# Kernel optimization log

Hardware: AMD Instinct MI355X
Metric: run time of the kernel (lower is better)

The kernel has to match this reference:

```python
import jax, jax.numpy as jnp
import numpy as np

N_HEAD = 12
LN_EPS = 1e-5


def _layernorm(x, g, b):
    m = jnp.mean(x, axis=-1, keepdims=True)
    v = jnp.mean(jnp.square(x - m), axis=-1, keepdims=True)
    return (x - m) * jax.lax.rsqrt(v + LN_EPS) * g + b


def _block(x, p):
    # p holds single-layer params. x: [B, S, D]
    B, S, D = x.shape
    Dh = D // N_HEAD
    h = _layernorm(x, p['ln1_g'], p['ln1_b'])
    q = (h @ p['wq'] + p['bq']).reshape(B, S, N_HEAD, Dh)
    k = (h @ p['wk'] + p['bk']).reshape(B, S, N_HEAD, Dh)
    v = (h @ p['wv'] + p['bv']).reshape(B, S, N_HEAD, Dh)
    scores = jnp.einsum('bqhd,bkhd->bhqk', q, k) / np.sqrt(Dh).astype(x.dtype)
    causal = jnp.tril(jnp.ones((S, S), dtype=bool))  # valid_nums = arange(1..S)
    scores = jnp.where(causal, scores, -jnp.inf)
    attn = jax.nn.softmax(scores, axis=-1)  # dropout is identity in eval
    o = jnp.einsum('bhqk,bkhd->bqhd', attn, v).reshape(B, S, D)
    x = x + o @ p['wo'] + p['bo']
    h2 = _layernorm(x, p['ln2_g'], p['ln2_b'])
    ff = jax.nn.gelu(h2 @ p['w1'] + p['b1'], approximate=False) @ p['w2'] + p['b2']
    return x + ff


def _gpt_forward(idx, wte, wpe, layer_params, lnf_g, lnf_b, lm_w):
    S = idx.shape[1]
    x = wte[idx] + wpe[None, :S, :]  # embd dropout is identity in eval
    x = jax.lax.scan(lambda c, p: (_block(c, p), None), x, layer_params)[0]
    x = _layernorm(x, lnf_g, lnf_b)
    return x @ lm_w  # logits [B, S, V]


def setup_inputs() -> dict:
    B, S, D, V, L, F = 4, 1024, 768, 50257, 12, 3072
    key = jax.random.key(0)
    ks = iter(jax.random.split(key, 24))
    std = 0.02
    std_proj = 0.02 / np.sqrt(2 * L)  # special init for w_o / FFN.linear2

    def w(shape, s=std):
        return jax.random.normal(next(ks), shape, jnp.float32) * s

    return dict(
        idx=jax.random.randint(next(ks), (B, S), 0, V),
        wte=w((V, D)), wpe=w((S, D)),
        ln1_g=jnp.ones((L, D)), ln1_b=jnp.zeros((L, D)),
        wq=w((L, D, D)), bq=jnp.zeros((L, D)),
        wk=w((L, D, D)), bk=jnp.zeros((L, D)),
        wv=w((L, D, D)), bv=jnp.zeros((L, D)),
        wo=w((L, D, D), std_proj), bo=jnp.zeros((L, D)),
        ln2_g=jnp.ones((L, D)), ln2_b=jnp.zeros((L, D)),
        w1=w((L, D, F)), b1=jnp.zeros((L, F)),
        w2=w((L, F, D), std_proj), b2=jnp.zeros((L, D)),
        lnf_g=jnp.ones((D,)), lnf_b=jnp.zeros((D,)),
        lm_w=w((D, V)),
    )


def reference(idx, wte, wpe, ln1_g, ln1_b, wq, bq, wk, bk, wv, bv, wo, bo,
              ln2_g, ln2_b, w1, b1, w2, b2, lnf_g, lnf_b, lm_w):
    layer_params = dict(ln1_g=ln1_g, ln1_b=ln1_b, wq=wq, bq=bq, wk=wk, bk=bk,
                        wv=wv, bv=bv, wo=wo, bo=bo, ln2_g=ln2_g, ln2_b=ln2_b,
                        w1=w1, b1=b1, w2=w2, b2=b2)
    return _gpt_forward(idx, wte, wpe, layer_params, lnf_g, lnf_b, lm_w)
```

## Files before the change

kernel.cpp:

```cpp
#include <hip/hip_runtime.h>
#include <hip/hip_bf16.h>

typedef __attribute__((ext_vector_type(8))) short short8;
typedef __attribute__((ext_vector_type(4))) float floatx4;

#define GLD16(g, l) __builtin_amdgcn_global_load_lds( \
    (__attribute__((address_space(1))) void*)(g),      \
    (__attribute__((address_space(3))) void*)(l), 16, 0, 0)

#define MFMA_BF16(a, b, c) __builtin_amdgcn_mfma_f32_16x16x32_bf16((a), (b), (c), 0, 0, 0)

__device__ __forceinline__ short f2bf(float f) {
  union { __hip_bfloat16 h; short s; } u;
  u.h = __float2bfloat16(f);
  return u.s;
}

__global__ __launch_bounds__(256)
void transpose_convert(const float* __restrict__ in, short* __restrict__ out,
                       const int K, const int N, const size_t inStride,
                       const size_t outStride) {
  in += blockIdx.z * inStride;
  out += blockIdx.z * outStride;
  __shared__ float tile[32][33];
  const int n0 = blockIdx.x * 32;
  const int k0 = blockIdx.y * 32;
  const int tx = threadIdx.x;
  const int ty = threadIdx.y;
#pragma unroll
  for (int i = 0; i < 4; ++i) {
    const int kk = ty + i * 8;
    const int nn = n0 + tx;
    tile[kk][tx] = (nn < N) ? in[(size_t)(k0 + kk) * N + nn] : 0.f;
  }
  __syncthreads();
#pragma unroll
  for (int i = 0; i < 4; ++i) {
    const int nn = ty + i * 8;
    out[(size_t)(n0 + nn) * K + k0 + tx] = f2bf(tile[tx][nn]);
  }
}

__global__ __launch_bounds__(256)
void embed_kernel(const int* __restrict__ idx, const float* __restrict__ wte,
                  const float* __restrict__ wpe, float* __restrict__ x) {
  const int row = blockIdx.x;
  const int tok = idx[row];
  const int s = row & 1023;
  const float* wt = wte + (size_t)tok * 768;
  const float* wp = wpe + (size_t)s * 768;
  float* xr = x + (size_t)row * 768;
  for (int c = threadIdx.x; c < 768; c += 256) xr[c] = wt[c] + wp[c];
}

__global__ __launch_bounds__(256)
void ln_kernel(const float* __restrict__ x, const float* __restrict__ g,
               const float* __restrict__ b, short* __restrict__ out) {
  const int row = blockIdx.x;
  const int t = threadIdx.x;
  const int wv = t >> 6, lane = t & 63;
  const float* xr = x + (size_t)row * 768;
  const float v0 = xr[t], v1 = xr[t + 256], v2 = xr[t + 512];
  __shared__ float red[4];
  float s = v0 + v1 + v2;
#pragma unroll
  for (int m = 1; m < 64; m <<= 1) s += __shfl_xor(s, m);
  if (lane == 0) red[wv] = s;
  __syncthreads();
  const float mean = (red[0] + red[1] + red[2] + red[3]) * (1.0f / 768.0f);
  __syncthreads();
  const float d0 = v0 - mean, d1 = v1 - mean, d2 = v2 - mean;
  float q = d0 * d0 + d1 * d1 + d2 * d2;
#pragma unroll
  for (int m = 1; m < 64; m <<= 1) q += __shfl_xor(q, m);
  if (lane == 0) red[wv] = q;
  __syncthreads();
  const float var = (red[0] + red[1] + red[2] + red[3]) * (1.0f / 768.0f);
  const float inv = rsqrtf(var + 1e-5f);
  short* orow = out + (size_t)row * 768;
  orow[t] = f2bf(d0 * inv * g[t] + b[t]);
  orow[t + 256] = f2bf(d1 * inv * g[t + 256] + b[t + 256]);
  orow[t + 512] = f2bf(d2 * inv * g[t + 512] + b[t + 512]);
}

enum { EPI_QKV = 0, EPI_RESID = 1, EPI_GELU = 2, EPI_LM = 3 };

template <int BM, int BN>
__device__ __forceinline__ void stage_tiles(const short* __restrict__ Ab,
                                            const short* __restrict__ Bb,
                                            const int K, const int kb,
                                            short* pa, short* pb,
                                            const int tid, const int wv) {
#pragma unroll
  for (int i = 0; i < BM / 32; ++i) {
    const int p = i * 256 + tid;
    const int rr = p >> 3, up = p & 7;
    GLD16(Ab + (size_t)rr * K + kb + ((up ^ (rr & 7)) << 3),
          pa + (i * 256 + wv * 64) * 8);
  }
#pragma unroll
  for (int i = 0; i < BN / 32; ++i) {
    const int p = i * 256 + tid;
    const int rr = p >> 3, up = p & 7;
    GLD16(Bb + (size_t)rr * K + kb + ((up ^ (rr & 7)) << 3),
          pb + (i * 256 + wv * 64) * 8);
  }
}

template <int BM, int BN, int EPI>
__global__ __launch_bounds__(256)
void gemm_kernel(const short* __restrict__ A, const short* __restrict__ Bt,
                 const int K,
                 const float* __restrict__ bias0, const float* __restrict__ bias1,
                 const float* __restrict__ bias2, float* __restrict__ fout,
                 short* __restrict__ bout0, short* __restrict__ bout1,
                 short* __restrict__ bout2) {
  constexpr int MF = BM / 32;
  constexpr int NF = BN / 32;
  __shared__ short sA[2][BM * 64];
  __shared__ short sB[2][BN * 64];
  const int tid = threadIdx.x;
  const int wv = tid >> 6;
  const int lane = tid & 63;
  const int lrow = lane & 15;
  const int lk8 = lane >> 4;
  const int m0 = blockIdx.x * BM;
  const int n0 = blockIdx.y * BN;
  const int wm = (wv >> 1) * (BM / 2);
  const int wn = (wv & 1) * (BN / 2);

  floatx4 acc[MF][NF];
#pragma unroll
  for (int m = 0; m < MF; ++m)
#pragma unroll
    for (int n = 0; n < NF; ++n) acc[m][n] = {0.f, 0.f, 0.f, 0.f};

  const short* Ab = A + (size_t)m0 * K;
  const short* Bb = Bt + (size_t)n0 * K;

  const int nk = K >> 6;
  stage_tiles<BM, BN>(Ab, Bb, K, 0, sA[0], sB[0], tid, wv);
  __syncthreads();

  int cur = 0;
  for (int kt = 0; kt < nk; ++kt) {
    if (kt + 1 < nk)
      stage_tiles<BM, BN>(Ab, Bb, K, (kt + 1) << 6, sA[cur ^ 1], sB[cur ^ 1],
                          tid, wv);
    const short* pa = sA[cur];
    const short* pb = sB[cur];
    short8 af[MF][2], bv[NF][2];
#pragma unroll
    for (int m = 0; m < MF; ++m)
#pragma unroll
      for (int ks = 0; ks < 2; ++ks)
        af[m][ks] = *(const short8*)(pa + (wm + m * 16 + lrow) * 64 +
                                     (((ks * 4 + lk8) ^ (lrow & 7)) << 3));
#pragma unroll
    for (int n = 0; n < NF; ++n)
#pragma unroll
      for (int ks = 0; ks < 2; ++ks)
        bv[n][ks] = *(const short8*)(pb + (wn + n * 16 + lrow) * 64 +
                                     (((ks * 4 + lk8) ^ (lrow & 7)) << 3));
#pragma unroll
    for (int m = 0; m < MF; ++m)
#pragma unroll
      for (int n = 0; n < NF; ++n) {
        acc[m][n] = MFMA_BF16(af[m][0], bv[n][0], acc[m][n]);
        acc[m][n] = MFMA_BF16(af[m][1], bv[n][1], acc[m][n]);
      }
    __syncthreads();
    cur ^= 1;
  }

#pragma unroll
  for (int m = 0; m < MF; ++m) {
#pragma unroll
    for (int n = 0; n < NF; ++n) {
#pragma unroll
      for (int r = 0; r < 4; ++r) {
        const float v = acc[m][n][r];
        const int gm = m0 + wm + m * 16 + lk8 * 4 + r;
        const int gn = n0 + wn + n * 16 + lrow;
        if (EPI == EPI_QKV) {
          const int sec = (gn >= 1536) ? 2 : (gn >= 768 ? 1 : 0);
          const int nn = gn - sec * 768;
          const int hh = nn >> 6, dh = nn & 63;
          const int bb = gm >> 10, srow = gm & 1023;
          if (sec == 0) {
            bout0[(((size_t)(bb * 12 + hh) * 1024 + srow) << 6) + dh] =
                f2bf((v + bias0[nn]) * 0.125f);
          } else if (sec == 1) {
            bout1[(((size_t)(bb * 12 + hh) * 1024 + srow) << 6) + dh] =
                f2bf(v + bias1[nn]);
          } else {
            bout2[(((size_t)(bb * 12 + hh) * 64 + dh) << 10) + srow] =
                f2bf(v + bias2[nn]);
          }
        } else if (EPI == EPI_RESID) {
          float* xp = fout + (size_t)gm * 768 + gn;
          *xp = *xp + v + bias0[gn];
        } else if (EPI == EPI_GELU) {
          const float tt = v + bias0[gn];
          const float gl = 0.5f * tt * (1.f + erff(tt * 0.70710678118654752f));
          bout0[(size_t)gm * 3072 + gn] = f2bf(gl);
        } else {
          if (gn < 50257) fout[(size_t)gm * 50257 + gn] = v;
        }
      }
    }
  }
}

__global__ __launch_bounds__(256)
void attn_kernel(const short* __restrict__ q, const short* __restrict__ k,
                 const short* __restrict__ vt, short* __restrict__ o) {
  __shared__ short sK[64 * 64];
  __shared__ short sV[64 * 64];
  __shared__ short sP[4][16 * 64];
  const int bh = blockIdx.x;
  const int qi = 15 - blockIdx.y;
  const int tid = threadIdx.x;
  const int wv = tid >> 6, lane = tid & 63;
  const int lrow = lane & 15, lk8 = lane >> 4;
  const int q0 = qi * 64;

  const short* qg = q + ((size_t)(bh * 1024 + q0 + wv * 16 + lrow)) * 64 + lk8 * 8;
  const short8 qf0 = *(const short8*)qg;
  const short8 qf1 = *(const short8*)(qg + 32);

  float m_run[4], lsum[4];
  floatx4 accO[4];
#pragma unroll
  for (int r = 0; r < 4; ++r) { m_run[r] = -1e30f; lsum[r] = 0.f; }
#pragma unroll
  for (int n = 0; n < 4; ++n) accO[n] = {0.f, 0.f, 0.f, 0.f};

  for (int t = 0; t <= qi; ++t) {
    const int k0 = t * 64;
#pragma unroll
    for (int i = 0; i < 2; ++i) {
      const int e = (i * 256 + tid) * 8;
      const int r = e >> 6, cc = e & 63;
      const int su = ((cc >> 3) ^ (r & 7)) << 3;
      *(short8*)(sK + r * 64 + su) =
          *(const short8*)(k + ((size_t)(bh * 1024 + k0 + r)) * 64 + cc);
      *(short8*)(sV + r * 64 + su) =
          *(const short8*)(vt + ((size_t)(bh * 64 + r)) * 1024 + k0 + cc);
    }
    __syncthreads();

    floatx4 accS[4];
#pragma unroll
    for (int n = 0; n < 4; ++n) accS[n] = {0.f, 0.f, 0.f, 0.f};
#pragma unroll
    for (int ks = 0; ks < 2; ++ks) {
      const short8 qf = ks ? qf1 : qf0;
      const int u = lk8 + ks * 4;
#pragma unroll
      for (int n = 0; n < 4; ++n) {
        const int key = n * 16 + lrow;
        const short8 kf = *(const short8*)(sK + key * 64 + ((u ^ (key & 7)) << 3));
        accS[n] = MFMA_BF16(qf, kf, accS[n]);
      }
    }

#pragma unroll
    for (int r = 0; r < 4; ++r) {
      const int qrow = q0 + wv * 16 + lk8 * 4 + r;
      float sv[4];
      float mx = -1e30f;
#pragma unroll
      for (int n = 0; n < 4; ++n) {
        float s = accS[n][r];
        const int key = k0 + n * 16 + lrow;
        s = (key > qrow) ? -1e30f : s;
        sv[n] = s;
        mx = fmaxf(mx, s);
      }
#pragma unroll
      for (int m = 1; m < 16; m <<= 1) mx = fmaxf(mx, __shfl_xor(mx, m));
      const float mnew = fmaxf(m_run[r], mx);
      const float sf = __expf(m_run[r] - mnew);
      m_run[r] = mnew;
      float rs = 0.f;
      const int prow = lk8 * 4 + r;
#pragma unroll
      for (int n = 0; n < 4; ++n) {
        const float pv = __expf(sv[n] - mnew);
        rs += pv;
        const int col = n * 16 + lrow;
        sP[wv][prow * 64 + (((col >> 3) ^ (prow & 7)) << 3) + (col & 7)] = f2bf(pv);
      }
#pragma unroll
      for (int m = 1; m < 16; m <<= 1) rs += __shfl_xor(rs, m);
      lsum[r] = lsum[r] * sf + rs;
#pragma unroll
      for (int n = 0; n < 4; ++n) accO[n][r] *= sf;
    }

#pragma unroll
    for (int ks = 0; ks < 2; ++ks) {
      const int u = lk8 + ks * 4;
      const short8 pf =
          *(const short8*)(&sP[wv][lrow * 64 + ((u ^ (lrow & 7)) << 3)]);
#pragma unroll
      for (int n = 0; n < 4; ++n) {
        const int dh = n * 16 + lrow;
        const short8 vf = *(const short8*)(sV + dh * 64 + ((u ^ (dh & 7)) << 3));
        accO[n] = MFMA_BF16(pf, vf, accO[n]);
      }
    }
    __syncthreads();
  }

  const int bb = bh / 12, hh = bh % 12;
#pragma unroll
  for (int n = 0; n < 4; ++n)
#pragma unroll
    for (int r = 0; r < 4; ++r) {
      const int row = q0 + wv * 16 + lk8 * 4 + r;
      const float ov = accO[n][r] / lsum[r];
      o[((size_t)(bb * 1024 + row)) * 768 + hh * 64 + n * 16 + lrow] = f2bf(ov);
    }
}

extern "C" void kernel_launch(void* const* d_in, const int* in_sizes, int n_in,
                              void* d_out, int out_size, void* d_ws, size_t ws_size,
                              hipStream_t stream) {
  const int* idx = (const int*)d_in[0];
  const float* wte = (const float*)d_in[1];
  const float* wpe = (const float*)d_in[2];
  const float* ln1_g = (const float*)d_in[3];
  const float* ln1_b = (const float*)d_in[4];
  const float* wq = (const float*)d_in[5];
  const float* bq = (const float*)d_in[6];
  const float* wk = (const float*)d_in[7];
  const float* bk = (const float*)d_in[8];
  const float* wv = (const float*)d_in[9];
  const float* bv = (const float*)d_in[10];
  const float* wo = (const float*)d_in[11];
  const float* bo = (const float*)d_in[12];
  const float* ln2_g = (const float*)d_in[13];
  const float* ln2_b = (const float*)d_in[14];
  const float* w1 = (const float*)d_in[15];
  const float* b1 = (const float*)d_in[16];
  const float* w2 = (const float*)d_in[17];
  const float* b2 = (const float*)d_in[18];
  const float* lnf_g = (const float*)d_in[19];
  const float* lnf_b = (const float*)d_in[20];
  const float* lm_w = (const float*)d_in[21];
  float* out = (float*)d_out;

  char* base = (char*)d_ws;
  size_t off = 0;
  auto alloc = [&](size_t bytes) {
    char* r = base + off;
    off = (off + bytes + 255) & ~(size_t)255;
    return r;
  };
  short* lmT = (short*)alloc((size_t)50304 * 768 * 2);
  float* x = (float*)alloc((size_t)4096 * 768 * 4);
  short* h = (short*)alloc((size_t)4096 * 768 * 2);
  short* qb = (short*)alloc((size_t)4096 * 768 * 2);
  short* kb = (short*)alloc((size_t)4096 * 768 * 2);
  short* vtb = (short*)alloc((size_t)4096 * 768 * 2);
  short* ob = (short*)alloc((size_t)4096 * 768 * 2);
  short* ff = (short*)alloc((size_t)4096 * 3072 * 2);

  const size_t LW = 7077888;
  const size_t dd = (size_t)768 * 768;
  const bool big = (off + (size_t)12 * LW * 2 + 256 <= ws_size);
  short* wAll = nullptr;
  short *wqkvT = nullptr, *woT = nullptr, *w1T = nullptr, *w2T = nullptr;
  if (big) {
    wAll = (short*)alloc((size_t)12 * LW * 2);
  } else {
    wqkvT = (short*)alloc((size_t)2304 * 768 * 2);
    woT = (short*)alloc((size_t)768 * 768 * 2);
    w1T = (short*)alloc((size_t)3072 * 768 * 2);
    w2T = (short*)alloc((size_t)768 * 3072 * 2);
    if (off > ws_size) return;
  }

  const dim3 tb(32, 8);
  transpose_convert<<<dim3(1572, 24, 1), tb, 0, stream>>>(lm_w, lmT, 768, 50257, 0, 0);
  if (big) {
    transpose_convert<<<dim3(24, 24, 12), tb, 0, stream>>>(wq, wAll + 0, 768, 768, dd, LW);
    transpose_convert<<<dim3(24, 24, 12), tb, 0, stream>>>(wk, wAll + 589824, 768, 768, dd, LW);
    transpose_convert<<<dim3(24, 24, 12), tb, 0, stream>>>(wv, wAll + 1179648, 768, 768, dd, LW);
    transpose_convert<<<dim3(24, 24, 12), tb, 0, stream>>>(wo, wAll + 1769472, 768, 768, dd, LW);
    transpose_convert<<<dim3(96, 24, 12), tb, 0, stream>>>(w1, wAll + 2359296, 768, 3072,
                                                           (size_t)768 * 3072, LW);
    transpose_convert<<<dim3(24, 96, 12), tb, 0, stream>>>(w2, wAll + 4718592, 3072, 768,
                                                           (size_t)3072 * 768, LW);
  }
  embed_kernel<<<4096, 256, 0, stream>>>(idx, wte, wpe, x);

  for (int l = 0; l < 12; ++l) {
    const short *pQKV, *pWO, *pW1, *pW2;
    if (big) {
      short* wl = wAll + (size_t)l * LW;
      pQKV = wl;
      pWO = wl + 1769472;
      pW1 = wl + 2359296;
      pW2 = wl + 4718592;
    } else {
      transpose_convert<<<dim3(24, 24, 1), tb, 0, stream>>>(wq + l * dd, wqkvT, 768, 768, 0, 0);
      transpose_convert<<<dim3(24, 24, 1), tb, 0, stream>>>(wk + l * dd, wqkvT + dd, 768, 768, 0, 0);
      transpose_convert<<<dim3(24, 24, 1), tb, 0, stream>>>(wv + l * dd, wqkvT + 2 * dd, 768, 768, 0, 0);
      transpose_convert<<<dim3(24, 24, 1), tb, 0, stream>>>(wo + l * dd, woT, 768, 768, 0, 0);
      transpose_convert<<<dim3(96, 24, 1), tb, 0, stream>>>(w1 + (size_t)l * 768 * 3072, w1T, 768, 3072, 0, 0);
      transpose_convert<<<dim3(24, 96, 1), tb, 0, stream>>>(w2 + (size_t)l * 3072 * 768, w2T, 3072, 768, 0, 0);
      pQKV = wqkvT; pWO = woT; pW1 = w1T; pW2 = w2T;
    }

    ln_kernel<<<4096, 256, 0, stream>>>(x, ln1_g + l * 768, ln1_b + l * 768, h);
    gemm_kernel<128, 64, EPI_QKV><<<dim3(32, 36), 256, 0, stream>>>(
        h, pQKV, 768, bq + l * 768, bk + l * 768, bv + l * 768, nullptr, qb, kb, vtb);
    attn_kernel<<<dim3(48, 16), 256, 0, stream>>>(qb, kb, vtb, ob);
    gemm_kernel<64, 64, EPI_RESID><<<dim3(64, 12), 256, 0, stream>>>(
        ob, pWO, 768, bo + l * 768, nullptr, nullptr, x, nullptr, nullptr, nullptr);
    ln_kernel<<<4096, 256, 0, stream>>>(x, ln2_g + l * 768, ln2_b + l * 768, h);
    gemm_kernel<128, 64, EPI_GELU><<<dim3(32, 48), 256, 0, stream>>>(
        h, pW1, 768, b1 + l * 3072, nullptr, nullptr, nullptr, ff, nullptr, nullptr);
    gemm_kernel<64, 64, EPI_RESID><<<dim3(64, 12), 256, 0, stream>>>(
        ff, pW2, 3072, b2 + l * 768, nullptr, nullptr, x, nullptr, nullptr, nullptr);
  }

  ln_kernel<<<4096, 256, 0, stream>>>(x, lnf_g, lnf_b, h);
  gemm_kernel<128, 128, EPI_LM><<<dim3(32, 393), 256, 0, stream>>>(
      h, lmT, 768, nullptr, nullptr, nullptr, out, nullptr, nullptr, nullptr);
}
```

Baseline: 3.271 ms.

## Add dedicated LM-head GEMM and register-resident softmax in attention

Replaces the generic 128x128 LM-head GEMM with a dedicated 512-thread kernel using 256x128 tiles and K fixed at 768. Restructures attention to compute S transposed (K·Q), so each lane owns one query row. The probabilities can then be packed into bf16 registers and fed straight into the PV MFMA, removing the shared-memory sP round trip and most cross-lane shuffles. It also switches to exp2f with log2e folded into the Q scale. The cost is more complex lane remapping of the rescale factors and higher register pressure in the new GEMM.

```diff
diff --git a/kernel.cpp b/kernel.cpp
--- a/kernel.cpp
+++ b/kernel.cpp
@@ -83,7 +83,7 @@
   orow[t + 512] = f2bf(d2 * inv * g[t + 512] + b[t + 512]);
 }
 
-enum { EPI_QKV = 0, EPI_RESID = 1, EPI_GELU = 2, EPI_LM = 3 };
+enum { EPI_QKV = 0, EPI_RESID = 1, EPI_GELU = 2 };
 
 template <int BM, int BN>
 __device__ __forceinline__ void stage_tiles(const short* __restrict__ Ab,
@@ -189,7 +189,7 @@
           const int bb = gm >> 10, srow = gm & 1023;
           if (sec == 0) {
             bout0[(((size_t)(bb * 12 + hh) * 1024 + srow) << 6) + dh] =
-                f2bf((v + bias0[nn]) * 0.125f);
+                f2bf((v + bias0[nn]) * 0.18033688f);
           } else if (sec == 1) {
             bout1[(((size_t)(bb * 12 + hh) * 1024 + srow) << 6) + dh] =
                 f2bf(v + bias1[nn]);
@@ -200,16 +200,103 @@
         } else if (EPI == EPI_RESID) {
           float* xp = fout + (size_t)gm * 768 + gn;
           *xp = *xp + v + bias0[gn];
-        } else if (EPI == EPI_GELU) {
+        } else {
           const float tt = v + bias0[gn];
           const float gl = 0.5f * tt * (1.f + erff(tt * 0.70710678118654752f));
           bout0[(size_t)gm * 3072 + gn] = f2bf(gl);
-        } else {
-          if (gn < 50257) fout[(size_t)gm * 50257 + gn] = v;
         }
       }
     }
   }
+}
+
+__global__ __launch_bounds__(512, 4)
+void gemm_lm_kernel(const short* __restrict__ A, const short* __restrict__ Bt,
+                    float* __restrict__ fout) {
+  __shared__ short sA[256 * 64];
+  __shared__ short sB[128 * 64];
+  const int K = 768;
+  const int tid = threadIdx.x;
+  const int wv = tid >> 6;
+  const int lane = tid & 63;
+  const int lrow = lane & 15;
+  const int lk8 = lane >> 4;
+  const int m0 = blockIdx.x * 256;
+  const int n0 = blockIdx.y * 128;
+  const int wm = (wv >> 1) * 64;
+  const int wn = (wv & 1) * 64;
+
+  floatx4 acc[4][4];
+#pragma unroll
+  for (int m = 0; m < 4; ++m)
+#pragma unroll
+    for (int n = 0; n < 4; ++n) acc[m][n] = {0.f, 0.f, 0.f, 0.f};
+
+  const short* Ab = A + (size_t)m0 * K;
+  const short* Bb = Bt + (size_t)n0 * K;
+
+  const short* pA[4];
+  const short* pB[2];
+#pragma unroll
+  for (int i = 0; i < 4; ++i) {
+    const int p = i * 512 + tid;
+    const int rr = p >> 3, up = p & 7;
+    pA[i] = Ab + (size_t)rr * K + ((up ^ (rr & 7)) << 3);
+  }
+#pragma unroll
+  for (int i = 0; i < 2; ++i) {
+    const int p = i * 512 + tid;
+    const int rr = p >> 3, up = p & 7;
+    pB[i] = Bb + (size_t)rr * K + ((up ^ (rr & 7)) << 3);
+  }
+
+  const int arow = (wm + lrow) * 64;
+  const int xr = (lrow & 7);
+
+  for (int kt = 0; kt < 12; ++kt) {
+#pragma unroll
+    for (int i = 0; i < 4; ++i) {
+      GLD16(pA[i], sA + (i * 512 + wv * 64) * 8);
+      pA[i] += 64;
+    }
+#pragma unroll
+    for (int i = 0; i < 2; ++i) {
+      GLD16(pB[i], sB + (i * 512 + wv * 64) * 8);
+      pB[i] += 64;
+    }
+    __syncthreads();
+
+    short8 bvv[4][2];
+#pragma unroll
+    for (int n = 0; n < 4; ++n) {
+      const int brow = (wn + n * 16 + lrow) * 64;
+      bvv[n][0] = *(const short8*)(sB + brow + ((lk8 ^ xr) << 3));
+      bvv[n][1] = *(const short8*)(sB + brow + (((4 + lk8) ^ xr) << 3));
+    }
+#pragma unroll
+    for (int m = 0; m < 4; ++m) {
+      const short8 a0 = *(const short8*)(sA + arow + m * 1024 + ((lk8 ^ xr) << 3));
+      const short8 a1 =
+          *(const short8*)(sA + arow + m * 1024 + (((4 + lk8) ^ xr) << 3));
+#pragma unroll
+      for (int n = 0; n < 4; ++n) {
+        acc[m][n] = MFMA_BF16(a0, bvv[n][0], acc[m][n]);
+        acc[m][n] = MFMA_BF16(a1, bvv[n][1], acc[m][n]);
+      }
+    }
+    __syncthreads();
+  }
+
+#pragma unroll
+  for (int m = 0; m < 4; ++m)
+#pragma unroll
+    for (int n = 0; n < 4; ++n)
+#pragma unroll
+      for (int r = 0; r < 4; ++r) {
+        const int gm = m0 + wm + m * 16 + lk8 * 4 + r;
+        const int gn = n0 + wn + n * 16 + lrow;
+        if (gn < 50257) fout[(size_t)gm * 50257 + gn] = acc[m][n][r];
+      }
 }
 
 __global__ __launch_bounds__(256)
@@ -217,22 +304,20 @@
                  const short* __restrict__ vt, short* __restrict__ o) {
   __shared__ short sK[64 * 64];
   __shared__ short sV[64 * 64];
-  __shared__ short sP[4][16 * 64];
   const int bh = blockIdx.x;
   const int qi = 15 - blockIdx.y;
   const int tid = threadIdx.x;
   const int wv = tid >> 6, lane = tid & 63;
   const int lrow = lane & 15, lk8 = lane >> 4;
   const int q0 = qi * 64;
-
-  const short* qg = q + ((size_t)(bh * 1024 + q0 + wv * 16 + lrow)) * 64 + lk8 * 8;
+  const int qrow = q0 + wv * 16 + lrow;
+
+  const short* qg = q + ((size_t)(bh * 1024 + qrow)) * 64 + lk8 * 8;
   const short8 qf0 = *(const short8*)qg;
   const short8 qf1 = *(const short8*)(qg + 32);
 
-  float m_run[4], lsum[4];
+  float m_run = -1e30f, lsum = 0.f;
   floatx4 accO[4];
-#pragma unroll
-  for (int r = 0; r < 4; ++r) { m_run[r] = -1e30f; lsum[r] = 0.f; }
 #pragma unroll
   for (int n = 0; n < 4; ++n) accO[n] = {0.f, 0.f, 0.f, 0.f};
 
@@ -253,66 +338,87 @@
     floatx4 accS[4];
 #pragma unroll
     for (int n = 0; n < 4; ++n) accS[n] = {0.f, 0.f, 0.f, 0.f};
+    const int rKb = ((lrow >> 2) << 3) + (lrow & 3);
 #pragma unroll
     for (int ks = 0; ks < 2; ++ks) {
       const short8 qf = ks ? qf1 : qf0;
-      const int u = lk8 + ks * 4;
 #pragma unroll
       for (int n = 0; n < 4; ++n) {
-        const int key = n * 16 + lrow;
-        const short8 kf = *(const short8*)(sK + key * 64 + ((u ^ (key & 7)) << 3));
-        accS[n] = MFMA_BF16(qf, kf, accS[n]);
-      }
-    }
-
-#pragma unroll
-    for (int r = 0; r < 4; ++r) {
-      const int qrow = q0 + wv * 16 + lk8 * 4 + r;
-      float sv[4];
-      float mx = -1e30f;
-#pragma unroll
-      for (int n = 0; n < 4; ++n) {
+        const int rK = ((n >> 1) << 5) + ((n & 1) << 2) + rKb;
+        const short8 kf =
+            *(const short8*)(sK + rK * 64 + (((ks * 4 + lk8) ^ (rK & 7)) << 3));
+        accS[n] = MFMA_BF16(kf, qf, accS[n]);
+      }
+    }
+
+    float sv[4][4];
+    float mx = -1e30f;
+#pragma unroll
+    for (int n = 0; n < 4; ++n)
+#pragma unroll
+      for (int r = 0; r < 4; ++r) {
+        const int key = k0 + ((n >> 1) << 5) + (lk8 << 3) + ((n & 1) << 2) + r;
         float s = accS[n][r];
-        const int key = k0 + n * 16 + lrow;
         s = (key > qrow) ? -1e30f : s;
-        sv[n] = s;
+        sv[n][r] = s;
         mx = fmaxf(mx, s);
       }
-#pragma unroll
-      for (int m = 1; m < 16; m <<= 1) mx = fmaxf(mx, __shfl_xor(mx, m));
-      const float mnew = fmaxf(m_run[r], mx);
-      const float sf = __expf(m_run[r] - mnew);
-      m_run[r] = mnew;
-      float rs = 0.f;
-      const int prow = lk8 * 4 + r;
-#pragma unroll
-      for (int n = 0; n < 4; ++n) {
-        const float pv = __expf(sv[n] - mnew);
-        rs += pv;
-        const int col = n * 16 + lrow;
-        sP[wv][prow * 64 + (((col >> 3) ^ (prow & 7)) << 3) + (col & 7)] = f2bf(pv);
-      }
-#pragma unroll
-      for (int m = 1; m < 16; m <<= 1) rs += __shfl_xor(rs, m);
-      lsum[r] = lsum[r] * sf + rs;
-#pragma unroll
-      for (int n = 0; n < 4; ++n) accO[n][r] *= sf;
-    }
-
-#pragma unroll
-    for (int ks = 0; ks < 2; ++ks) {
-      const int u = lk8 + ks * 4;
-      const short8 pf =
-          *(const short8*)(&sP[wv][lrow * 64 + ((u ^ (lrow & 7)) << 3)]);
-#pragma unroll
-      for (int n = 0; n < 4; ++n) {
-        const int dh = n * 16 + lrow;
-        const short8 vf = *(const short8*)(sV + dh * 64 + ((u ^ (dh & 7)) << 3));
-        accO[n] = MFMA_BF16(pf, vf, accO[n]);
-      }
+    mx = fmaxf(mx, __shfl_xor(mx, 16));
+    mx = fmaxf(mx, __shfl_xor(mx, 32));
+    const float mnew = fmaxf(m_run, mx);
+    const float sf = exp2f(m_run - mnew);
+    m_run = mnew;
+
+    float rs = 0.f;
+    unsigned int w[4][2];
+#pragma unroll
+    for (int n = 0; n < 4; ++n)
+#pragma unroll
+      for (int rp = 0; rp < 2; ++rp) {
+        const float ea = exp2f(sv[n][2 * rp] - mnew);
+        const float eb = exp2f(sv[n][2 * rp + 1] - mnew);
+        rs += ea + eb;
+        w[n][rp] = (unsigned int)(unsigned short)f2bf(ea) |
+                   ((unsigned int)(unsigned short)f2bf(eb) << 16);
+      }
+    lsum = lsum * sf + rs;
+
+    float sfq[4];
+#pragma unroll
+    for (int r = 0; r < 4; ++r)
+      sfq[r] = __shfl(sf, (lane & 48) | (lk8 * 4 + r));
+#pragma unroll
+    for (int n = 0; n < 4; ++n)
+#pragma unroll
+      for (int r = 0; r < 4; ++r) accO[n][r] *= sfq[r];
+
+    union { short8 s; unsigned int u[4]; } paf0, paf1;
+#pragma unroll
+    for (int tt = 0; tt < 4; ++tt) {
+      paf0.u[tt] = w[tt >> 1][tt & 1];
+      paf1.u[tt] = w[2 + (tt >> 1)][tt & 1];
+    }
+
+#pragma unroll
+    for (int n = 0; n < 4; ++n) {
+      const int dh = n * 16 + lrow;
+      const short8 vf0 = *(const short8*)(sV + dh * 64 + ((lk8 ^ (dh & 7)) << 3));
+      const short8 vf1 =
+          *(const short8*)(sV + dh * 64 + (((4 + lk8) ^ (dh & 7)) << 3));
+      accO[n] = MFMA_BF16(paf0.s, vf0, accO[n]);
+      accO[n] = MFMA_BF16(paf1.s, vf1, accO[n]);
     }
     __syncthreads();
   }
+
+  float ls = lsum;
+  ls += __shfl_xor(ls, 16);
+  ls += __shfl_xor(ls, 32);
+  const float invown = 1.f / ls;
+  float invq[4];
+#pragma unroll
+  for (int r = 0; r < 4; ++r)
+    invq[r] = __shfl(invown, (lane & 48) | (lk8 * 4 + r));
 
   const int bb = bh / 12, hh = bh % 12;
 #pragma unroll
@@ -320,7 +426,7 @@
 #pragma unroll
     for (int r = 0; r < 4; ++r) {
       const int row = q0 + wv * 16 + lk8 * 4 + r;
-      const float ov = accO[n][r] / lsum[r];
+      const float ov = accO[n][r] * invq[r];
       o[((size_t)(bb * 1024 + row)) * 768 + hh * 64 + n * 16 + lrow] = f2bf(ov);
     }
 }
@@ -429,6 +535,5 @@
   }
 
   ln_kernel<<<4096, 256, 0, stream>>>(x, lnf_g, lnf_b, h);
-  gemm_kernel<128, 128, EPI_LM><<<dim3(32, 393), 256, 0, stream>>>(
-      h, lmT, 768, nullptr, nullptr, nullptr, out, nullptr, nullptr, nullptr);
-}
+  gemm_lm_kernel<<<dim3(16, 393), 512, 0, stream>>>(h, lmT, out);
+}
```

New measurement: 2.886 ms. 1.13x faster.
